# Kernel optimization log

Hardware: AMD Instinct MI355X
Metric: run time of the kernel (lower is better)

Reference implementation:

```python
import jax, jax.numpy as jnp
import numpy as np

B, H0, W0, C0 = 4, 60, 60, 256
HEADS, WS, WSS, KWS = 8, 7, 3, 27
NEG = -1000.0


def layer_norm(x, g, b, eps=1e-5):
    m = jnp.mean(x, -1, keepdims=True)
    v = jnp.mean((x - m) ** 2, -1, keepdims=True)
    return (x - m) * jax.lax.rsqrt(v + eps) * g + b


def setup_inputs() -> dict:
    key = jax.random.key(0)
    ks = jax.random.split(key, 10)
    w = lambda k, shape: jax.random.normal(k, shape, jnp.float32) * 0.02
    ns = ((H0 + (WS - H0 % WS) % WS) // WS) * WSS  # 27 semantic tokens per dim
    return {
        "x": jax.random.normal(ks[0], (B, H0 * W0, C0), jnp.float32),
        "y": jax.random.normal(ks[1], (B, ns * ns, C0), jnp.float32),
        "norm1_g": jnp.ones((C0,), jnp.float32),
        "norm1_b": jnp.zeros((C0,), jnp.float32),
        "q_w": w(ks[2], (C0, C0)),
        "kv_w": w(ks[3], (C0, 2 * C0)),
        "proj_w": w(ks[4], (C0, C0)),
        "proj_b": jnp.zeros((C0,), jnp.float32),
        "norm2_g": jnp.ones((C0,), jnp.float32),
        "norm2_b": jnp.zeros((C0,), jnp.float32),
        "fc1_w": w(ks[5], (C0, 4 * C0)),
        "fc1_b": jnp.zeros((4 * C0,), jnp.float32),
        "fc2_w": w(ks[6], (4 * C0, C0)),
        "fc2_b": jnp.zeros((C0,), jnp.float32),
        "ls1": jax.random.normal(ks[7], (C0,), jnp.float32) * 0.1,
        "ls2": jax.random.normal(ks[8], (C0,), jnp.float32) * 0.1,
        "H": H0,
        "W": W0,
    }


def reference(x, y, norm1_g, norm1_b, q_w, kv_w, proj_w, proj_b,
              norm2_g, norm2_b, fc1_w, fc1_b, fc2_w, fc2_b, ls1, ls2, H, W):
    Bsz, L, C = x.shape
    hd = C // HEADS
    pad_r = (WS - W % WS) % WS
    pad_b = (WS - H % WS) % WS
    Hp, Wp = H + pad_b, W + pad_r
    nWh, nWw = Hp // WS, Wp // WS
    # ---- window-partition image queries: [B*nWh*nWw, WS*WS, C]
    xi = jnp.pad(x.reshape(Bsz, H, W, C), ((0, 0), (0, pad_b), (0, pad_r), (0, 0)))
    xw = xi.reshape(Bsz, nWh, WS, nWw, WS, C).transpose(0, 1, 3, 2, 4, 5).reshape(-1, WS * WS, C)
    shortcut = xw
    xn = layer_norm(xw, norm1_g, norm1_b)
    # ---- overlapping key windows from semantic tokens (unfold kernel=KWS, stride=WSS)
    ns0, ns1 = nWh * WSS, nWw * WSS
    left = (KWS - WSS) // 2
    right = KWS - WSS - left
    yp = jnp.pad(y.reshape(Bsz, ns0, ns1, C), ((0, 0), (left, right), (left, right), (0, 0)))
    idh = jnp.arange(nWh)[:, None] * WSS + jnp.arange(KWS)[None, :]  # [nWh, KWS]
    idw = jnp.arange(nWw)[:, None] * WSS + jnp.arange(KWS)[None, :]
    kwin = yp[:, idh[:, None, :, None], idw[None, :, None, :], :]  # [B,nWh,nWw,KWS,KWS,C]
    kwin = layer_norm(kwin.reshape(-1, KWS * KWS, C), norm1_g, norm1_b)
    # ---- pad mask: bottom-right padded corner + out-of-grid key positions
    m = jnp.zeros((Bsz, ns0, ns1), x.dtype)
    m = m.at[:, ns0 - pad_b:, ns1 - pad_r:].set(NEG)
    m = jnp.pad(m, ((0, 0), (left, right), (left, right)), constant_values=NEG)
    mwin = m[:, idh[:, None, :, None], idw[None, :, None, :]].reshape(-1, 1, 1, KWS * KWS)
    # ---- cross attention: queries 49 tokens, keys 729 tokens per window
    q = (xn @ q_w).reshape(-1, WS * WS, HEADS, hd).transpose(0, 2, 1, 3)
    kv = (kwin @ kv_w).reshape(-1, KWS * KWS, 2, HEADS, hd)
    k = kv[:, :, 0].transpose(0, 2, 1, 3)
    v = kv[:, :, 1].transpose(0, 2, 1, 3)
    attn = jax.nn.softmax(jnp.einsum('whqd,whkd->whqk', q, k) * (hd ** -0.5) + mwin, axis=-1)
    o = jnp.einsum('whqk,whkd->whqd', attn, v).transpose(0, 2, 1, 3).reshape(-1, WS * WS, C)
    o = o @ proj_w + proj_b
    xw = shortcut + ls1 * o
    # ---- merge windows, crop away padding
    xo = xw.reshape(Bsz, nWh, nWw, WS, WS, C).transpose(0, 1, 3, 2, 4, 5).reshape(Bsz, Hp, Wp, C)
    xo = xo[:, :H, :W, :].reshape(Bsz, H * W, C)
    # ---- MLP with layer-scale residual
    h = layer_norm(xo, norm2_g, norm2_b)
    h = jax.nn.gelu(h @ fc1_w + fc1_b, approximate=False) @ fc2_w + fc2_b
    return xo + ls2 * h
```

## Files before the change

kernel.cpp:

```cpp
#include <hip/hip_runtime.h>
#include <hip/hip_bf16.h>

typedef __hip_bfloat16 bf16;
typedef __attribute__((ext_vector_type(8))) short bf16x8;
typedef __attribute__((ext_vector_type(4))) float f32x4;


#define QSCALE 0.25505402616302864f

__device__ __forceinline__ bf16 f2bf(float f){ return __float2bfloat16(f); }
__device__ __forceinline__ unsigned short f2bfu(float f){
  __hip_bfloat16 h = __float2bfloat16(f);
  return *(unsigned short*)&h;
}
__device__ __forceinline__ float fexp2(float x){
  float r; asm("v_exp_f32 %0, %1" : "=v"(r) : "v"(x)); return r;
}
__device__ __forceinline__ unsigned cvtpk(float lo, float hi){
  unsigned r; asm("v_cvt_pk_bf16_f32 %0, %1, %2" : "=v"(r) : "v"(lo), "v"(hi));
  return r;
}

__global__ __launch_bounds__(256) void wt_kernel(
    const float* __restrict__ fc1_w, const float* __restrict__ fc2_w,
    const float* __restrict__ proj_w, const float* __restrict__ q_w,
    const float* __restrict__ kv_w,
    bf16* __restrict__ W1F, bf16* __restrict__ W2F, bf16* __restrict__ PWF,
    bf16* __restrict__ QWF, bf16* __restrict__ KVF, bf16* __restrict__ vbufT,
    float* __restrict__ maskbuf){
  int gid = blockIdx.x*256 + threadIdx.x;
  if (gid < 262144){
    int e=gid&7, lane=(gid>>3)&63, kc=(gid>>9)&7, nt=gid>>12;
    int li=lane&15, lg=lane>>4;
    W1F[gid] = f2bf(fc1_w[(size_t)(kc*32+lg*8+e)*1024 + nt*16+li]);
  } else if (gid < 524288){
    int o = gid - 262144;
    int e=o&7, lane=(o>>3)&63, kc=(o>>9)&31, nt=o>>14;
    int li=lane&15, lg=lane>>4;
    W2F[o] = f2bf(fc2_w[(size_t)(kc*32+lg*8+e)*256 + nt*16+li]);
  } else if (gid < 589824){
    int o = gid - 524288;
    int e=o&7, lane=(o>>3)&63, kc=(o>>9)&7, nt=o>>12;
    int li=lane&15, lg=lane>>4;
    PWF[o] = f2bf(proj_w[(size_t)(kc*32+lg*8+e)*256 + nt*16+li]);
  } else if (gid < 655360){
    int o = gid - 589824;
    int e=o&7, lane=(o>>3)&63, kc=(o>>9)&7, nt=o>>12;
    int li=lane&15, lg=lane>>4;
    QWF[o] = f2bf(q_w[(size_t)(kc*32+lg*8+e)*256 + nt*16+li] * QSCALE);
  } else if (gid < 786432){
    int o = gid - 655360;
    int e=o&7, lane=(o>>3)&63, kc=(o>>9)&7, nt=o>>12;
    int li=lane&15, lg=lane>>4;
    KVF[o] = f2bf(kv_w[(size_t)(kc*32+lg*8+e)*512 + nt*16+li]);
  } else {
    int idx = gid - 786432;
    if (idx < 7168){
      int row = idx/7, p = idx - row*7;
      vbufT[(size_t)row*736 + 729 + p] = f2bf(0.f);
    } else if (idx < 7680){
      vbufT[(size_t)1024*736 + (idx-7168)] = f2bf(0.f);
    } else {
      int o = idx - 7680;
      int wi2 = o / 768, local = o - wi2*768;
      int wh2 = wi2/9, ww2 = wi2 - wh2*9;
      int C2 = 81*wh2 + 3*ww2 - 336;
      int off2 = C2 & 7;
      int kk = local - off2;
      bool valid = ((unsigned)kk < 729u);
      int kr = valid ? kk/27 : 0;
      int kc2 = kk - kr*27;
      int gr = wh2*3 - 12 + kr, gc = ww2*3 - 12 + kc2;
      valid = valid && ((unsigned)gr < 27u) && ((unsigned)gc < 27u)
                    && !(gr >= 24 && gc >= 24);
      maskbuf[(size_t)wi2*768 + local] = valid ? 0.f : -30000.f;
    }
  }
}

__global__ __launch_bounds__(256) void kvq_kernel(
    const float* __restrict__ y, const float* __restrict__ x,
    const float* __restrict__ g, const float* __restrict__ bb,
    const bf16* __restrict__ KVF, const bf16* __restrict__ QWF,
    bf16* __restrict__ kbuf, bf16* __restrict__ vbufT, bf16* __restrict__ qbuf){
  __shared__ __align__(16) unsigned short xn[16*256];
  int tid = threadIdx.x, wid = tid>>6, lane = tid&63;
  int li = lane&15, lg = lane>>4;
  if (blockIdx.x < 366){
    int blk = blockIdx.x;
    int tok0 = (blk >> 1) * 16;
    int half = blk & 1;
    {
      float4 g4 = ((const float4*)g)[lane];
      float4 b4 = ((const float4*)bb)[lane];
      #pragma unroll
      for (int tt=0; tt<4; tt++){
        int t = wid*4 + tt;
        int gtok = tok0 + t;
        float4 v = make_float4(0.f,0.f,0.f,0.f);
        if (gtok < 2916) v = ((const float4*)(y + (size_t)gtok*256))[lane];
        float s = v.x+v.y+v.z+v.w, ss = v.x*v.x+v.y*v.y+v.z*v.z+v.w*v.w;
        #pragma unroll
        for (int off=32; off; off>>=1){ s += __shfl_xor(s,off); ss += __shfl_xor(ss,off); }
        float mean = s*(1.f/256.f);
        float var  = fmaxf(ss*(1.f/256.f) - mean*mean, 0.f);
        float inv  = rsqrtf(var + 1e-5f);
        ushort4 pk;
        pk.x = f2bfu((v.x-mean)*inv*g4.x+b4.x);
        pk.y = f2bfu((v.y-mean)*inv*g4.y+b4.y);
        pk.z = f2bfu((v.z-mean)*inv*g4.z+b4.z);
        pk.w = f2bfu((v.w-mean)*inv*g4.w+b4.w);
        int idx = (t*256 + lane*4) ^ ((t&7)<<3);
        *(ushort4*)&xn[idx] = pk;
      }
    }
    __syncthreads();
    bf16x8 a[8];
    #pragma unroll
    for (int ks=0; ks<8; ks++){
      int idx = (li*256 + ks*32 + lg*8) ^ ((li&7)<<3);
      a[ks] = *(const bf16x8*)&xn[idx];
    }
    #pragma unroll
    for (int nn=0; nn<4; nn++){
      int ntg = half*16 + wid*4 + nn;
      const bf16* wp = KVF + (size_t)ntg*4096 + lane*8;
      f32x4 acc = {0.f,0.f,0.f,0.f};
      #pragma unroll
      for (int ks=0; ks<8; ks++){
        bf16x8 bfrag = *(const bf16x8*)(wp + ks*512);
        acc = __builtin_amdgcn_mfma_f32_16x16x32_bf16(a[ks], bfrag, acc, 0, 0, 0);
      }
      int col = ntg*16 + li;
      #pragma unroll
      for (int r=0; r<4; r++){
        int tok = tok0 + lg*4 + r;
        if (tok < 2916){
          if (col < 256){
            kbuf[(size_t)tok*256 + col] = f2bf(acc[r]);
          } else {
            int b2 = (tok>=729) + (tok>=1458) + (tok>=2187);
            int ltok = tok - b2*729;
            vbufT[(size_t)(b2*256 + col-256)*736 + ltok] = f2bf(acc[r]);
          }
        }
      }
    }
  } else {
    int row0 = (blockIdx.x - 366) * 16;
    {
      float4 g4 = ((const float4*)g)[lane];
      float4 b4 = ((const float4*)bb)[lane];
      #pragma unroll
      for (int tt=0; tt<4; tt++){
        int t = wid*4 + tt;
        int row = row0 + t;
        float4 v = make_float4(0.f,0.f,0.f,0.f);
        if (row < 15876){
          int w = row/49, t2 = row - w*49;
          int b = w/81, wi = w - b*81;
          int wh = wi/9, ww = wi - wh*9;
          int r = t2/7, c = t2 - r*7;
          int gh = wh*7 + r, gw = ww*7 + c;
          if (gh < 60 && gw < 60)
            v = ((const float4*)(x + (size_t)(b*3600 + gh*60 + gw)*256))[lane];
        }
        float s=v.x+v.y+v.z+v.w, ss=v.x*v.x+v.y*v.y+v.z*v.z+v.w*v.w;
        #pragma unroll
        for (int off=32; off; off>>=1){ s += __shfl_xor(s,off); ss += __shfl_xor(ss,off); }
        float mean = s*(1.f/256.f);
        float var = fmaxf(ss*(1.f/256.f)-mean*mean, 0.f);
        float inv = rsqrtf(var+1e-5f);
        ushort4 pk;
        pk.x = f2bfu((v.x-mean)*inv*g4.x+b4.x);
        pk.y = f2bfu((v.y-mean)*inv*g4.y+b4.y);
        pk.z = f2bfu((v.z-mean)*inv*g4.z+b4.z);
        pk.w = f2bfu((v.w-mean)*inv*g4.w+b4.w);
        int idx = (t*256 + lane*4) ^ ((t&7)<<3);
        *(ushort4*)&xn[idx] = pk;
      }
    }
    __syncthreads();
    bf16x8 a[8];
    #pragma unroll
    for (int ks=0; ks<8; ks++){
      int idx = (li*256 + ks*32 + lg*8) ^ ((li&7)<<3);
      a[ks] = *(const bf16x8*)&xn[idx];
    }
    #pragma unroll
    for (int nt=0; nt<4; nt++){
      int ntg = wid*4 + nt;
      const bf16* wp = QWF + (size_t)ntg*4096 + lane*8;
      f32x4 acc = {0.f,0.f,0.f,0.f};
      #pragma unroll
      for (int ks=0; ks<8; ks++){
        bf16x8 bfrag = *(const bf16x8*)(wp + ks*512);
        acc = __builtin_amdgcn_mfma_f32_16x16x32_bf16(a[ks], bfrag, acc, 0, 0, 0);
      }
      int col = ntg*16 + li;
      #pragma unroll
      for (int r=0; r<4; r++){
        int row = row0 + lg*4 + r;
        if (row < 15876)
          qbuf[(size_t)row*256 + col] = f2bf(acc[r]);
      }
    }
  }
}

__global__ __launch_bounds__(512) void attn_kernel(
    const bf16* __restrict__ qbuf, const bf16* __restrict__ kbuf,
    const bf16* __restrict__ vbufT, const float* __restrict__ maskbuf,
    bf16* __restrict__ obuf){
  __shared__ __align__(16) unsigned short Kls[2][4096];
  __shared__ __align__(16) unsigned short VlsF[2][8192];

  int tid = threadIdx.x;
  int sub = tid >> 8;
  int t256 = tid & 255;
  int wid = t256 >> 6, lane = tid & 63;
  int lg = lane>>4, li = lane&15;
  int blk = (blockIdx.x & 7)*162 + (blockIdx.x >> 3);
  int w = blk >> 2, hp = blk & 3;
  int hh = hp*2 + sub;
  int b = w/81, wi = w - b*81, wh = wi/9, ww = wi - wh*9;

  int C  = 81*wh + 3*ww - 336;
  int T0 = C & ~7, off = C & 7;
  int kr_min = 12 - 3*wh; if (kr_min < 0) kr_min = 0;
  int kr_max = 39 - 3*wh; if (kr_max > 27) kr_max = 27;
  int t0 = (kr_min*27 + off) >> 7;
  int t1 = (kr_max*27 + off + 127) >> 7;

  const bf16* kb  = kbuf  + (long long)(b*729 + T0)*256 + hh*32;
  const bf16* vbT = vbufT + (long long)(b*256 + hh*32)*736 + T0;
  const float* mk = maskbuf + wi*768;

  const bf16* ksrcA = kb + (long long)(2*wid*16 + li)*256 + lg*8;
  const bf16* ksrcB = kb + (long long)((2*wid+1)*16 + li)*256 + lg*8;
  int vrow = t256>>4, vch = t256&15;
  const bf16* vsrcA = vbT + (long long)vrow*736 + vch*8;
  const bf16* vsrcB = vbT + (long long)(vrow+16)*736 + vch*8;
  int vc_ = vch>>2, vhalf = (vch>>1)&1, vlg0 = (vch&1)*2;
  unsigned vdst0 = (unsigned)(((vc_*64 + vlg0*16     + vrow)*16 + vhalf*8) ^ (vc_<<5));
  unsigned vdst1 = (unsigned)(((vc_*64 + (vlg0+1)*16 + vrow)*16 + vhalf*8) ^ (vc_<<5));
  char* Vbase = (char*)&VlsF[sub][0];
  unsigned short* Kbase = &Kls[sub][0];

  bf16x8 qf;
  #pragma unroll
  for (int e=0;e<8;e++) qf[e]=0;
  int qrow = wid*16 + li;
  if (qrow < 49)
    qf = *(const bf16x8*)(qbuf + ((size_t)w*49+qrow)*256 + hh*32 + lg*8);

  f32x4 o0 = {0.f,0.f,0.f,0.f}, o1 = {0.f,0.f,0.f,0.f};
  float m = -3.0e38f, l = 0.f;

  {
    int j0 = t0*128;
    uint4 k0 = *(const uint4*)(ksrcA + (long long)j0*256);
    uint4 k1 = *(const uint4*)(ksrcB + (long long)j0*256);
    uint4 v0 = *(const uint4*)(vsrcA + j0);
    uint4 v1 = *(const uint4*)(vsrcB + j0);
    *(uint4*)&Kbase[2*wid*512 + lane*8]     = k0;
    *(uint4*)&Kbase[(2*wid+1)*512 + lane*8] = k1;
    *(uint2*)(Vbase + vdst0)        = make_uint2(v0.x, v0.y);
    *(uint2*)(Vbase + vdst1)        = make_uint2(v0.z, v0.w);
    *(uint2*)(Vbase + 8192 + vdst0) = make_uint2(v1.x, v1.y);
    *(uint2*)(Vbase + 8192 + vdst1) = make_uint2(v1.z, v1.w);
  }
  __syncthreads();

  for (int tile=t0; tile<t1; tile++){
    int jbase = tile*128;
    uint4 nk0, nk1, nv0, nv1;
    if (tile+1 < t1){
      int jn = jbase + 128;
      nk0 = *(const uint4*)(ksrcA + (long long)jn*256);
      nk1 = *(const uint4*)(ksrcB + (long long)jn*256);
      nv0 = *(const uint4*)(vsrcA + jn);
      nv1 = *(const uint4*)(vsrcB + jn);
    }
    __builtin_amdgcn_s_setprio(1);
    f32x4 s[8];
    #pragma unroll
    for (int t=0;t<8;t++){
      bf16x8 kf = *(const bf16x8*)&Kbase[t*512 + lane*8];
      float4 mv = *(const float4*)(mk + jbase + t*16 + lg*4);
      f32x4 cin = {mv.x, mv.y, mv.z, mv.w};
      s[t] = __builtin_amdgcn_mfma_f32_16x16x32_bf16(kf, qf, cin, 0, 0, 0);
    }
    float m0 = fmaxf(fmaxf(s[0][0], s[0][1]), fmaxf(s[0][2], s[0][3]));
    float m1 = fmaxf(fmaxf(s[1][0], s[1][1]), fmaxf(s[1][2], s[1][3]));
    float m2 = fmaxf(fmaxf(s[2][0], s[2][1]), fmaxf(s[2][2], s[2][3]));
    float m3 = fmaxf(fmaxf(s[3][0], s[3][1]), fmaxf(s[3][2], s[3][3]));
    float m4 = fmaxf(fmaxf(s[4][0], s[4][1]), fmaxf(s[4][2], s[4][3]));
    float m5 = fmaxf(fmaxf(s[5][0], s[5][1]), fmaxf(s[5][2], s[5][3]));
    float m6 = fmaxf(fmaxf(s[6][0], s[6][1]), fmaxf(s[6][2], s[6][3]));
    float m7 = fmaxf(fmaxf(s[7][0], s[7][1]), fmaxf(s[7][2], s[7][3]));
    float mt = fmaxf(fmaxf(fmaxf(m0, m1), fmaxf(m2, m3)),
                     fmaxf(fmaxf(m4, m5), fmaxf(m6, m7)));
    mt = fmaxf(mt, __shfl_xor(mt, 16));
    mt = fmaxf(mt, __shfl_xor(mt, 32));
    if (!__all(mt - m <= 8.f)){
      float mn = fmaxf(m, mt);
      float fac = fexp2(m - mn);
      m = mn;
      l *= fac;
      #pragma unroll
      for (int r=0;r<4;r++){ o0[r] *= fac; o1[r] *= fac; }
    }
    float ps = 0.f;
    #pragma unroll
    for (int t=0;t<8;t++){
      #pragma unroll
      for (int r=0;r<4;r++){
        float p = fexp2(s[t][r] - m);
        s[t][r] = p;
        ps += p;
      }
    }
    ps += __shfl_xor(ps, 16);
    ps += __shfl_xor(ps, 32);
    l += ps;
    unsigned pk[8][2];
    #pragma unroll
    for (int t=0;t<8;t++){
      pk[t][0] = cvtpk(s[t][0], s[t][1]);
      pk[t][1] = cvtpk(s[t][2], s[t][3]);
    }
    #pragma unroll
    for (int c=0;c<4;c++){
      union { unsigned u[4]; bf16x8 v; } pb;
      pb.u[0]=pk[2*c][0];   pb.u[1]=pk[2*c][1];
      pb.u[2]=pk[2*c+1][0]; pb.u[3]=pk[2*c+1][1];
      unsigned offb = (unsigned)(((c*64 + lg*16 + li)*16) ^ (c<<5));
      bf16x8 va = *(const bf16x8*)(Vbase + offb);
      bf16x8 vcf = *(const bf16x8*)(Vbase + 8192 + offb);
      o0 = __builtin_amdgcn_mfma_f32_16x16x32_bf16(va,  pb.v, o0, 0, 0, 0);
      o1 = __builtin_amdgcn_mfma_f32_16x16x32_bf16(vcf, pb.v, o1, 0, 0, 0);
    }
    __builtin_amdgcn_s_setprio(0);
    if (tile+1 < t1){
      __syncthreads();
      *(uint4*)&Kbase[2*wid*512 + lane*8]     = nk0;
      *(uint4*)&Kbase[(2*wid+1)*512 + lane*8] = nk1;
      *(uint2*)(Vbase + vdst0)        = make_uint2(nv0.x, nv0.y);
      *(uint2*)(Vbase + vdst1)        = make_uint2(nv0.z, nv0.w);
      *(uint2*)(Vbase + 8192 + vdst0) = make_uint2(nv1.x, nv1.y);
      *(uint2*)(Vbase + 8192 + vdst1) = make_uint2(nv1.z, nv1.w);
      __syncthreads();
    }
  }

  if (qrow < 49){
    float rl = 1.f / l;
    bf16* op = obuf + ((size_t)w*49 + qrow)*256 + hh*32;
    unsigned da0 = cvtpk(o0[0]*rl, o0[1]*rl);
    unsigned da1 = cvtpk(o0[2]*rl, o0[3]*rl);
    unsigned db0 = cvtpk(o1[0]*rl, o1[1]*rl);
    unsigned db1 = cvtpk(o1[2]*rl, o1[3]*rl);
    *(uint2*)(op + lg*4)      = make_uint2(da0, da1);
    *(uint2*)(op + 16 + lg*4) = make_uint2(db0, db1);
  }
}

__global__ __launch_bounds__(256) void proj_kernel(
    const bf16* __restrict__ obuf, const float* __restrict__ x,
    const bf16* __restrict__ PWF, const float* __restrict__ proj_b,
    const float* __restrict__ ls1, float* __restrict__ xobuf){
  int tid = threadIdx.x, wid = tid>>6, lane = tid&63;
  int li = lane&15, lg = lane>>4;
  int row0 = blockIdx.x * 16;
  int rowA = row0 + li; if (rowA > 15875) rowA = 15875;
  bf16x8 a[8];
  #pragma unroll
  for (int ks=0; ks<8; ks++)
    a[ks] = *(const bf16x8*)(obuf + (size_t)rowA*256 + ks*32 + lg*8);
  float pbv[4], l1v[4];
  #pragma unroll
  for (int nt=0; nt<4; nt++){
    int col = wid*64 + nt*16 + li;
    pbv[nt] = proj_b[col];
    l1v[nt] = ls1[col];
  }
  f32x4 acc[4];
  #pragma unroll
  for (int nt=0; nt<4; nt++){
    const bf16* wp = PWF + (size_t)(wid*4 + nt)*4096 + lane*8;
    f32x4 z = {0.f,0.f,0.f,0.f};
    #pragma unroll
    for (int ks=0; ks<8; ks++){
      bf16x8 bfrag = *(const bf16x8*)(wp + ks*512);
      z = __builtin_amdgcn_mfma_f32_16x16x32_bf16(a[ks], bfrag, z, 0, 0, 0);
    }
    acc[nt] = z;
  }
  #pragma unroll
  for (int r=0; r<4; r++){
    int row = row0 + lg*4 + r;
    if (row < 15876){
      int w = row/49, t2 = row - w*49;
      int b = w/81, wi = w - b*81;
      int wh = wi/9, ww = wi - wh*9;
      int r2 = t2/7, c2 = t2 - r2*7;
      int gh = wh*7 + r2, gw = ww*7 + c2;
      if (gh < 60 && gw < 60){
        size_t base = (size_t)(b*3600 + gh*60 + gw)*256;
        #pragma unroll
        for (int nt=0; nt<4; nt++){
          int col = wid*64 + nt*16 + li;
          xobuf[base + col] = x[base + col] + l1v[nt]*(acc[nt][r] + pbv[nt]);
        }
      }
    }
  }
}

__global__ __launch_bounds__(256) void mlp_kernel(
    const float* __restrict__ xobuf, const float* __restrict__ g,
    const float* __restrict__ bb, const bf16* __restrict__ W1F,
    const float* __restrict__ fc1_b, const bf16* __restrict__ W2F,
    const float* __restrict__ fc2_b, const float* __restrict__ ls2,
    float* __restrict__ out){
  __shared__ __align__(16) unsigned short xn[16*256];
  __shared__ __align__(16) unsigned short Hls[16*1024];
  int tid = threadIdx.x, wid = tid>>6, lane = tid&63;
  int li = lane&15, lg = lane>>4;
  int tok0 = blockIdx.x * 16;
  {
    float4 g4 = ((const float4*)g)[lane];
    float4 b4 = ((const float4*)bb)[lane];
    #pragma unroll
    for (int tt=0; tt<4; tt++){
      int t = wid*4 + tt;
      float4 v = ((const float4*)(xobuf + (size_t)(tok0+t)*256))[lane];
      float s = v.x+v.y+v.z+v.w;
      float ss = v.x*v.x+v.y*v.y+v.z*v.z+v.w*v.w;
      #pragma unroll
      for (int off=32; off; off>>=1){ s += __shfl_xor(s,off); ss += __shfl_xor(ss,off); }
      float mean = s*(1.f/256.f);
      float var = fmaxf(ss*(1.f/256.f)-mean*mean, 0.f);
      float inv = rsqrtf(var+1e-5f);
      ushort4 pk;
      pk.x = f2bfu((v.x-mean)*inv*g4.x+b4.x);
      pk.y = f2bfu((v.y-mean)*inv*g4.y+b4.y);
      pk.z = f2bfu((v.z-mean)*inv*g4.z+b4.z);
      pk.w = f2bfu((v.w-mean)*inv*g4.w+b4.w);
      int idx = (t*256 + lane*4) ^ ((t&7)<<3);
      *(ushort4*)&xn[idx] = pk;
    }
  }
  __syncthreads();
  bf16x8 a1[8];
  #pragma unroll
  for (int ks=0; ks<8; ks++){
    int idx = (li*256 + ks*32 + lg*8) ^ ((li&7)<<3);
    a1[ks] = *(const bf16x8*)&xn[idx];
  }
  const bf16* w1base = W1F + (size_t)(wid*16)*4096 + lane*8;
  bf16x8 bcur[8], bnxt[8];
  #pragma unroll
  for (int ks=0; ks<8; ks++) bcur[ks] = *(const bf16x8*)(w1base + ks*512);
  #pragma unroll 4
  for (int nn=0; nn<16; nn++){
    if (nn < 15){
      const bf16* wpn = w1base + (size_t)(nn+1)*4096;
      #pragma unroll
      for (int ks=0; ks<8; ks++) bnxt[ks] = *(const bf16x8*)(wpn + ks*512);
    }
    f32x4 hc = {0.f,0.f,0.f,0.f};
    #pragma unroll
    for (int ks=0; ks<8; ks++)
      hc = __builtin_amdgcn_mfma_f32_16x16x32_bf16(a1[ks], bcur[ks], hc, 0, 0, 0);
    int ntg = wid*16 + nn;
    float bias = fc1_b[ntg*16 + li];
    int col = ntg*16 + li;
    #pragma unroll
    for (int r=0; r<4; r++){
      float h = hc[r] + bias;
      float z = 0.7978845608f*(h + 0.044715f*h*h*h);
      z = fminf(fmaxf(z, -15.f), 15.f);
      float e = __expf(2.f*z);
      float gv = 0.5f*h*(1.f + (e-1.f)/(e+1.f));
      int row = lg*4 + r;
      int idx = (row*1024 + col) ^ ((row&7)<<3);
      Hls[idx] = f2bfu(gv);
    }
    #pragma unroll
    for (int ks=0; ks<8; ks++) bcur[ks] = bnxt[ks];
  }
  __syncthreads();
  f32x4 oacc[4];
  #pragma unroll
  for (int nt=0; nt<4; nt++) oacc[nt] = (f32x4){0.f,0.f,0.f,0.f};
  bf16x8 hcur, hnxt, b2c[4], b2n[4];
  {
    int idx = (li*1024 + lg*8) ^ ((li&7)<<3);
    hcur = *(const bf16x8*)&Hls[idx];
    #pragma unroll
    for (int nt=0; nt<4; nt++)
      b2c[nt] = *(const bf16x8*)(W2F + ((size_t)(wid*4+nt)*32)*512 + lane*8);
  }
  #pragma unroll 4
  for (int kc=0; kc<32; kc++){
    if (kc < 31){
      int idx = (li*1024 + (kc+1)*32 + lg*8) ^ ((li&7)<<3);
      hnxt = *(const bf16x8*)&Hls[idx];
      #pragma unroll
      for (int nt=0; nt<4; nt++)
        b2n[nt] = *(const bf16x8*)(W2F + ((size_t)(wid*4+nt)*32 + kc+1)*512 + lane*8);
    }
    #pragma unroll
    for (int nt=0; nt<4; nt++)
      oacc[nt] = __builtin_amdgcn_mfma_f32_16x16x32_bf16(hcur, b2c[nt], oacc[nt], 0, 0, 0);
    hcur = hnxt;
    #pragma unroll
    for (int nt=0; nt<4; nt++) b2c[nt] = b2n[nt];
  }
  #pragma unroll
  for (int nt=0; nt<4; nt++){
    int col = wid*64 + nt*16 + li;
    float l2 = ls2[col];
    float cb = fc2_b[col];
    #pragma unroll
    for (int r=0; r<4; r++){
      int tok = tok0 + lg*4 + r;
      size_t p = (size_t)tok*256 + col;
      out[p] = xobuf[p] + l2*(oacc[nt][r] + cb);
    }
  }
}

extern "C" void kernel_launch(void* const* d_in, const int* in_sizes, int n_in,
                              void* d_out, int out_size, void* d_ws, size_t ws_size,
                              hipStream_t stream) {
  (void)in_sizes; (void)n_in; (void)out_size; (void)ws_size;
  const float* x      = (const float*)d_in[0];
  const float* y      = (const float*)d_in[1];
  const float* n1g    = (const float*)d_in[2];
  const float* n1b    = (const float*)d_in[3];
  const float* q_w    = (const float*)d_in[4];
  const float* kv_w   = (const float*)d_in[5];
  const float* proj_w = (const float*)d_in[6];
  const float* proj_b = (const float*)d_in[7];
  const float* n2g    = (const float*)d_in[8];
  const float* n2b    = (const float*)d_in[9];
  const float* fc1_w  = (const float*)d_in[10];
  const float* fc1_b  = (const float*)d_in[11];
  const float* fc2_w  = (const float*)d_in[12];
  const float* fc2_b  = (const float*)d_in[13];
  const float* ls1    = (const float*)d_in[14];
  const float* ls2    = (const float*)d_in[15];

  char* ws = (char*)d_ws;
  bf16*  qbuf  = (bf16*)(ws);
  bf16*  kbuf  = (bf16*)(ws + 8128512);
  bf16*  vbufT = (bf16*)(ws + 9621504);
  bf16*  obuf  = (bf16*)(ws + 14745600);
  float* xobuf = (float*)(ws);
  bf16*  W1F   = (bf16*)(ws + 22874112);
  bf16*  W2F   = (bf16*)(ws + 23398400);
  bf16*  PWF   = (bf16*)(ws + 23922688);
  bf16*  QWF   = (bf16*)(ws + 24053760);
  bf16*  KVF   = (bf16*)(ws + 24184832);
  float* maskbuf = (float*)(ws + 24446976);

  wt_kernel<<<3345, 256, 0, stream>>>(fc1_w, fc2_w, proj_w, q_w, kv_w,
                                      W1F, W2F, PWF, QWF, KVF, vbufT, maskbuf);
  kvq_kernel<<<1359, 256, 0, stream>>>(y, x, n1g, n1b, KVF, QWF,
                                       kbuf, vbufT, qbuf);
  attn_kernel<<<1296, 512, 0, stream>>>(qbuf, kbuf, vbufT, maskbuf, obuf);
  proj_kernel<<<993, 256, 0, stream>>>(obuf, x, PWF, proj_b, ls1, xobuf);
  mlp_kernel<<<900, 256, 0, stream>>>(xobuf, n2g, n2b, W1F, fc1_b, W2F, fc2_b, ls2,
                                      (float*)d_out);
}
```

Measured before the change: 126.6 us.

## Fuse projection and MLP kernels into one per-pixel-tile kernel

Merges the output projection with the residual and the MLP into a single kernel that works on 16-pixel tiles in image order, gathering attention output rows by computing each pixel's window index. The intermediate xo tile lives in shared memory (aliased with the hidden buffer) and in registers instead of a global fp32 buffer, which removes one launch and a full write and read of the xo tensor. The cost is higher register and LDS pressure and scattered gathers from obuf, which may reduce occupancy.

```diff
diff --git a/kernel.cpp b/kernel.cpp
--- a/kernel.cpp
+++ b/kernel.cpp
@@ -366,26 +366,44 @@
   }
 }
 
-__global__ __launch_bounds__(256) void proj_kernel(
+__global__ __launch_bounds__(256) void projmlp_kernel(
     const bf16* __restrict__ obuf, const float* __restrict__ x,
     const bf16* __restrict__ PWF, const float* __restrict__ proj_b,
-    const float* __restrict__ ls1, float* __restrict__ xobuf){
+    const float* __restrict__ ls1,
+    const float* __restrict__ g, const float* __restrict__ bb,
+    const bf16* __restrict__ W1F, const float* __restrict__ fc1_b,
+    const bf16* __restrict__ W2F, const float* __restrict__ fc2_b,
+    const float* __restrict__ ls2, float* __restrict__ out){
+  __shared__ __align__(16) unsigned short xn[16*256];
+  __shared__ __align__(16) char ubuf[32768];
+  float* xo_ls = (float*)ubuf;
+  unsigned short* Hls = (unsigned short*)ubuf;
   int tid = threadIdx.x, wid = tid>>6, lane = tid&63;
   int li = lane&15, lg = lane>>4;
-  int row0 = blockIdx.x * 16;
-  int rowA = row0 + li; if (rowA > 15875) rowA = 15875;
+  int pix0 = blockIdx.x * 16;
+
   bf16x8 a[8];
-  #pragma unroll
-  for (int ks=0; ks<8; ks++)
-    a[ks] = *(const bf16x8*)(obuf + (size_t)rowA*256 + ks*32 + lg*8);
-  float pbv[4], l1v[4];
+  {
+    int pixA = pix0 + li;
+    int b = pixA/3600, rem = pixA - b*3600;
+    int gh = rem/60, gw = rem - gh*60;
+    int w = b*81 + (gh/7)*9 + (gw/7);
+    int t = (gh%7)*7 + (gw%7);
+    long long wrow = (long long)w*49 + t;
+    #pragma unroll
+    for (int ks=0; ks<8; ks++)
+      a[ks] = *(const bf16x8*)(obuf + wrow*256 + ks*32 + lg*8);
+  }
+  float pbv[4], l1v[4], l2v[4], cbv[4];
   #pragma unroll
   for (int nt=0; nt<4; nt++){
     int col = wid*64 + nt*16 + li;
     pbv[nt] = proj_b[col];
     l1v[nt] = ls1[col];
-  }
-  f32x4 acc[4];
+    l2v[nt] = ls2[col];
+    cbv[nt] = fc2_b[col];
+  }
+  float xov[4][4];
   #pragma unroll
   for (int nt=0; nt<4; nt++){
     const bf16* wp = PWF + (size_t)(wid*4 + nt)*4096 + lane*8;
@@ -395,47 +413,22 @@
       bf16x8 bfrag = *(const bf16x8*)(wp + ks*512);
       z = __builtin_amdgcn_mfma_f32_16x16x32_bf16(a[ks], bfrag, z, 0, 0, 0);
     }
-    acc[nt] = z;
-  }
-  #pragma unroll
-  for (int r=0; r<4; r++){
-    int row = row0 + lg*4 + r;
-    if (row < 15876){
-      int w = row/49, t2 = row - w*49;
-      int b = w/81, wi = w - b*81;
-      int wh = wi/9, ww = wi - wh*9;
-      int r2 = t2/7, c2 = t2 - r2*7;
-      int gh = wh*7 + r2, gw = ww*7 + c2;
-      if (gh < 60 && gw < 60){
-        size_t base = (size_t)(b*3600 + gh*60 + gw)*256;
-        #pragma unroll
-        for (int nt=0; nt<4; nt++){
-          int col = wid*64 + nt*16 + li;
-          xobuf[base + col] = x[base + col] + l1v[nt]*(acc[nt][r] + pbv[nt]);
-        }
-      }
-    }
-  }
-}
-
-__global__ __launch_bounds__(256) void mlp_kernel(
-    const float* __restrict__ xobuf, const float* __restrict__ g,
-    const float* __restrict__ bb, const bf16* __restrict__ W1F,
-    const float* __restrict__ fc1_b, const bf16* __restrict__ W2F,
-    const float* __restrict__ fc2_b, const float* __restrict__ ls2,
-    float* __restrict__ out){
-  __shared__ __align__(16) unsigned short xn[16*256];
-  __shared__ __align__(16) unsigned short Hls[16*1024];
-  int tid = threadIdx.x, wid = tid>>6, lane = tid&63;
-  int li = lane&15, lg = lane>>4;
-  int tok0 = blockIdx.x * 16;
+    int col = wid*64 + nt*16 + li;
+    #pragma unroll
+    for (int r=0; r<4; r++){
+      float xo = x[(size_t)(pix0 + lg*4 + r)*256 + col] + l1v[nt]*(z[r] + pbv[nt]);
+      xov[nt][r] = xo;
+      xo_ls[(lg*4 + r)*260 + col] = xo;
+    }
+  }
+  __syncthreads();
   {
     float4 g4 = ((const float4*)g)[lane];
     float4 b4 = ((const float4*)bb)[lane];
     #pragma unroll
     for (int tt=0; tt<4; tt++){
       int t = wid*4 + tt;
-      float4 v = ((const float4*)(xobuf + (size_t)(tok0+t)*256))[lane];
+      float4 v = *(const float4*)&xo_ls[t*260 + lane*4];
       float s = v.x+v.y+v.z+v.w;
       float ss = v.x*v.x+v.y*v.y+v.z*v.z+v.w*v.w;
       #pragma unroll
@@ -522,13 +515,10 @@
   #pragma unroll
   for (int nt=0; nt<4; nt++){
     int col = wid*64 + nt*16 + li;
-    float l2 = ls2[col];
-    float cb = fc2_b[col];
     #pragma unroll
     for (int r=0; r<4; r++){
-      int tok = tok0 + lg*4 + r;
-      size_t p = (size_t)tok*256 + col;
-      out[p] = xobuf[p] + l2*(oacc[nt][r] + cb);
+      size_t p = (size_t)(pix0 + lg*4 + r)*256 + col;
+      out[p] = xov[nt][r] + l2v[nt]*(oacc[nt][r] + cbv[nt]);
     }
   }
 }
@@ -559,7 +549,6 @@
   bf16*  kbuf  = (bf16*)(ws + 8128512);
   bf16*  vbufT = (bf16*)(ws + 9621504);
   bf16*  obuf  = (bf16*)(ws + 14745600);
-  float* xobuf = (float*)(ws);
   bf16*  W1F   = (bf16*)(ws + 22874112);
   bf16*  W2F   = (bf16*)(ws + 23398400);
   bf16*  PWF   = (bf16*)(ws + 23922688);
@@ -572,7 +561,7 @@
   kvq_kernel<<<1359, 256, 0, stream>>>(y, x, n1g, n1b, KVF, QWF,
                                        kbuf, vbufT, qbuf);
   attn_kernel<<<1296, 512, 0, stream>>>(qbuf, kbuf, vbufT, maskbuf, obuf);
-  proj_kernel<<<993, 256, 0, stream>>>(obuf, x, PWF, proj_b, ls1, xobuf);
-  mlp_kernel<<<900, 256, 0, stream>>>(xobuf, n2g, n2b, W1F, fc1_b, W2F, fc2_b, ls2,
-                                      (float*)d_out);
-}
+  projmlp_kernel<<<900, 256, 0, stream>>>(obuf, x, PWF, proj_b, ls1,
+                                          n2g, n2b, W1F, fc1_b, W2F, fc2_b, ls2,
+                                          (float*)d_out);
+}
```

Result: faster. 121.7 us (-3.8%).
